# Kernel tuning notes

Measured on AMD Instinct MI355X. Metric: run time of the kernel, lower is better.

Reference implementation:

```python
import jax, jax.numpy as jnp
import numpy as np

IN_D = 4096
OUT_D = 4096
NNZ = 1677722
BATCH = 4096
NEG_SLOPE = 0.1


def setup_inputs() -> dict:
    key = jax.random.key(0)
    k_x, k_w, k_b, k_r, k_c = jax.random.split(key, 5)
    x = jax.random.normal(k_x, (BATCH, IN_D), dtype=jnp.float32)
    weight = jax.random.normal(k_w, (NNZ,), dtype=jnp.float32)
    bias = jax.random.normal(k_b, (OUT_D,), dtype=jnp.float32)
    rows = jax.random.randint(k_r, (NNZ,), 0, IN_D, dtype=jnp.int32)
    cols = jax.random.randint(k_c, (NNZ,), 0, OUT_D, dtype=jnp.int32)
    return {"x": x, "weight": weight, "bias": bias, "rows": rows, "cols": cols}


def reference(x, weight, bias, rows, cols):
    # Sparse.forward: W = zeros(in_d, out_d); W[loc] = weight; rho(bias + x @ W)
    W = jnp.zeros((IN_D, OUT_D), dtype=x.dtype).at[rows, cols].set(weight)
    return jax.nn.leaky_relu(bias + x @ W, negative_slope=NEG_SLOPE)
```

## Files before the change

### kernel.cpp

```cpp
#include <hip/hip_runtime.h>
#include <stdint.h>

#define IN_D  4096
#define OUT_D 4096
#define BATCH 4096
#define NEG_SLOPE 0.1f
#define NSEG 8
#define SEGCAP 192

typedef __attribute__((ext_vector_type(8))) short short8;
typedef __attribute__((ext_vector_type(4))) float f32x4;

__device__ __forceinline__ unsigned short f2bf(float f) {
    unsigned u = __builtin_bit_cast(unsigned, f);
    u += 0x7FFFu + ((u >> 16) & 1u);
    return (unsigned short)(u >> 16);
}

__device__ __forceinline__ void gload_lds16(const unsigned short* gsrc, unsigned short* ldsp) {
    __builtin_amdgcn_global_load_lds(
        (const __attribute__((address_space(1))) unsigned int*)gsrc,
        (__attribute__((address_space(3))) unsigned int*)ldsp,
        16, 0, 0);
}

__global__ void zerocnt_kernel(uint4* __restrict__ cnt4) {
    int i = blockIdx.x * blockDim.x + threadIdx.x;
    cnt4[i] = make_uint4(0u, 0u, 0u, 0u);
}

__global__ void bucketcvt_kernel(const int* __restrict__ rows, const int* __restrict__ cols,
                                 const float* __restrict__ w,
                                 unsigned* __restrict__ cnt, uint2* __restrict__ bucket,
                                 int nnz,
                                 const float4* __restrict__ x, ushort4* __restrict__ xb,
                                 int nx4) {
    const int stride = gridDim.x * blockDim.x;
    const int i0 = blockIdx.x * blockDim.x + threadIdx.x;
    const int g = blockIdx.x & (NSEG - 1);
    for (int i = i0; i < nnz; i += stride) {
        int c = cols[i];
        unsigned pos = atomicAdd(&cnt[g * OUT_D + c], 1u);
        if (pos < SEGCAP)
            bucket[((size_t)g * OUT_D + c) * SEGCAP + pos] =
                make_uint2((unsigned)rows[i] | ((unsigned)f2bf(w[i]) << 16),
                           (unsigned)(i + 1));
    }
    for (int i = i0; i < nx4; i += stride) {
        float4 v = x[i];
        ushort4 o;
        o.x = f2bf(v.x); o.y = f2bf(v.y); o.z = f2bf(v.z); o.w = f2bf(v.w);
        xb[i] = o;
    }
}

__global__ __launch_bounds__(256) void coldedup_kernel(
        const uint2* __restrict__ bucket, const unsigned* __restrict__ cnt,
        unsigned short* __restrict__ Wt) {
    __shared__ unsigned tag[IN_D];
    __shared__ unsigned short wv[IN_D];
    const int col = blockIdx.x;
    const int tid = threadIdx.x;

    for (int r = tid; r < IN_D; r += 256) tag[r] = 0u;
    __syncthreads();

    #pragma unroll
    for (int g = 0; g < NSEG; ++g) {
        const int n = min((int)cnt[g * OUT_D + col], SEGCAP);
        const uint2* bk = bucket + ((size_t)g * OUT_D + col) * SEGCAP;
        for (int e = tid; e < n; e += 256) {
            uint2 u = bk[e];
            atomicMax(&tag[u.x & 0xFFFu], u.y);
        }
    }
    __syncthreads();
    #pragma unroll
    for (int g = 0; g < NSEG; ++g) {
        const int n = min((int)cnt[g * OUT_D + col], SEGCAP);
        const uint2* bk = bucket + ((size_t)g * OUT_D + col) * SEGCAP;
        for (int e = tid; e < n; e += 256) {
            uint2 u = bk[e];
            if (tag[u.x & 0xFFFu] == u.y) wv[u.x & 0xFFFu] = (unsigned short)(u.x >> 16);
        }
    }
    __syncthreads();

    const int r0 = tid * 16;
    short8 o0, o1;
    #pragma unroll
    for (int j = 0; j < 8; ++j) {
        o0[j] = tag[r0 + j]     ? (short)wv[r0 + j]     : (short)0;
        o1[j] = tag[r0 + 8 + j] ? (short)wv[r0 + 8 + j] : (short)0;
    }
    *(short8*)&Wt[(size_t)col * IN_D + r0]     = o0;
    *(short8*)&Wt[(size_t)col * IN_D + r0 + 8] = o1;
}

#define BM 256
#define BN 256
#define BK 64
#define NT (IN_D / BK)

#define QUAD(MI0, NI0, BREG) \
    _Pragma("unroll") \
    for (int mi = 0; mi < 4; ++mi) { \
      _Pragma("unroll") \
      for (int ni = 0; ni < 2; ++ni) { \
        _Pragma("unroll") \
        for (int ks = 0; ks < 2; ++ks) { \
          acc[(MI0)+mi][(NI0)+ni] = __builtin_amdgcn_mfma_f32_16x16x32_bf16( \
              a[mi][ks], BREG[ni][ks], acc[(MI0)+mi][(NI0)+ni], 0, 0, 0); \
        } } }

#define PHASE_TAIL(QUADCALL) \
    __builtin_amdgcn_s_barrier(); \
    asm volatile("s_waitcnt lgkmcnt(0)" ::: "memory"); \
    __builtin_amdgcn_sched_barrier(0); \
    __builtin_amdgcn_s_setprio(1); \
    QUADCALL; \
    __builtin_amdgcn_s_setprio(0); \
    __builtin_amdgcn_s_barrier();

__global__ __launch_bounds__(512) void gemm_kernel(
        const unsigned short* __restrict__ Xb,
        const unsigned short* __restrict__ Wt,
        const float* __restrict__ bias,
        float* __restrict__ out)
{
    __shared__ unsigned short lds[2][2][2][128 * 64];

    const int tid  = threadIdx.x;
    const int lane = tid & 63;
    const int wave = tid >> 6;

    const int lin = blockIdx.y * 16 + blockIdx.x;
    const int swz = (lin & 7) * 32 + (lin >> 3);
    const int m0 = (swz >> 4) * BM;
    const int n0 = (swz & 15) * BN;

    const int wm = (wave >> 2) * 128;
    const int wn = (wave & 3) * 64;

    const int lr = lane & 15;
    const int kg = lane >> 4;
    const int x7 = lr & 7;
    const int l8 = lane >> 3;
    const int c8 = lane & 7;

    const int kp0 = ((0 * 4 + kg) ^ x7) * 8;
    const int kp1 = ((1 * 4 + kg) ^ x7) * 8;

    const int jA_base = (wave >> 2) * 64 + lr;
    int jB[4];
    #pragma unroll
    for (int ni = 0; ni < 4; ++ni) {
        int r16 = wn + ni * 16;
        jB[ni] = (r16 & 31) + ((r16 >> 6) << 5) + lr;
    }

    auto stageA = [&](int d, int h, int kt) {
        #pragma unroll
        for (int s = 0; s < 2; ++s) {
            int j = wave * 16 + s * 8 + l8;
            int trow = (j & 63) + h * 64 + ((j >> 6) << 7);
            const unsigned short* src =
                Xb + (size_t)(m0 + trow) * IN_D + kt * BK + 8 * (c8 ^ l8);
            gload_lds16(src, &lds[d][0][h][(wave * 16 + s * 8) * 64]);
        }
    };
    auto stageB = [&](int d, int h, int kt) {
        #pragma unroll
        for (int s = 0; s < 2; ++s) {
            int j = wave * 16 + s * 8 + l8;
            int trow = (j & 31) + h * 32 + ((j >> 5) << 6);
            const unsigned short* src =
                Wt + (size_t)(n0 + trow) * IN_D + kt * BK + 8 * (c8 ^ l8);
            gload_lds16(src, &lds[d][1][h][(wave * 16 + s * 8) * 64]);
        }
    };

    f32x4 acc[8][4] = {};
    short8 a[4][2], b0[2][2], b1[2][2];

    stageA(0, 0, 0); stageB(0, 0, 0); stageB(0, 1, 0); stageA(0, 1, 0);
    stageA(1, 0, 1); stageB(1, 1, 1); stageA(1, 1, 1);
    asm volatile("s_waitcnt vmcnt(6)" ::: "memory");
    __builtin_amdgcn_s_barrier();
    #pragma unroll
    for (int mi = 0; mi < 4; ++mi) {
        a[mi][0] = *(const short8*)&lds[0][0][0][(jA_base + mi * 16) * 64 + kp0];
        a[mi][1] = *(const short8*)&lds[0][0][0][(jA_base + mi * 16) * 64 + kp1];
    }
    b0[0][0] = *(const short8*)&lds[0][1][0][jB[0] * 64 + kp0];
    b0[0][1] = *(const short8*)&lds[0][1][0][jB[0] * 64 + kp1];
    b0[1][0] = *(const short8*)&lds[0][1][0][jB[1] * 64 + kp0];
    b0[1][1] = *(const short8*)&lds[0][1][0][jB[1] * 64 + kp1];

    for (int t = 0; t < NT; ++t) {
        const int cur = t & 1, nxt = cur ^ 1;
        const int kt1 = (t + 1) & (NT - 1);
        const int kt2 = (t + 2) & (NT - 1);

        stageB(nxt, 0, kt1);
        PHASE_TAIL(QUAD(0, 0, b0))

        b1[0][0] = *(const short8*)&lds[cur][1][1][jB[2] * 64 + kp0];
        b1[0][1] = *(const short8*)&lds[cur][1][1][jB[2] * 64 + kp1];
        b1[1][0] = *(const short8*)&lds[cur][1][1][jB[3] * 64 + kp0];
        b1[1][1] = *(const short8*)&lds[cur][1][1][jB[3] * 64 + kp1];
        stageA(cur, 0, kt2);
        PHASE_TAIL(QUAD(0, 2, b1))

        #pragma unroll
        for (int mi = 0; mi < 4; ++mi) {
            a[mi][0] = *(const short8*)&lds[cur][0][1][(jA_base + mi * 16) * 64 + kp0];
            a[mi][1] = *(const short8*)&lds[cur][0][1][(jA_base + mi * 16) * 64 + kp1];
        }
        stageB(cur, 1, kt2);
        PHASE_TAIL(QUAD(4, 2, b1))

        stageA(cur, 1, kt2);
        asm volatile("s_waitcnt vmcnt(6)" ::: "memory");
        __builtin_amdgcn_s_barrier();
        asm volatile("s_waitcnt lgkmcnt(0)" ::: "memory");
        __builtin_amdgcn_sched_barrier(0);
        __builtin_amdgcn_s_setprio(1);
        QUAD(4, 0, b0)
        __builtin_amdgcn_s_setprio(0);
        #pragma unroll
        for (int mi = 0; mi < 4; ++mi) {
            a[mi][0] = *(const short8*)&lds[nxt][0][0][(jA_base + mi * 16) * 64 + kp0];
            a[mi][1] = *(const short8*)&lds[nxt][0][0][(jA_base + mi * 16) * 64 + kp1];
        }
        b0[0][0] = *(const short8*)&lds[nxt][1][0][jB[0] * 64 + kp0];
        b0[0][1] = *(const short8*)&lds[nxt][1][0][jB[0] * 64 + kp1];
        b0[1][0] = *(const short8*)&lds[nxt][1][0][jB[1] * 64 + kp0];
        b0[1][1] = *(const short8*)&lds[nxt][1][0][jB[1] * 64 + kp1];
        __builtin_amdgcn_s_barrier();
    }

    float bfrag[4];
    #pragma unroll
    for (int ni = 0; ni < 4; ++ni) bfrag[ni] = bias[n0 + wn + ni * 16 + lr];

    #pragma unroll
    for (int mi = 0; mi < 8; ++mi) {
        #pragma unroll
        for (int ni = 0; ni < 4; ++ni) {
            const int col = n0 + wn + ni * 16 + lr;
            #pragma unroll
            for (int r = 0; r < 4; ++r) {
                const int row = m0 + wm + mi * 16 + kg * 4 + r;
                float v = acc[mi][ni][r] + bfrag[ni];
                v = v > 0.0f ? v : v * NEG_SLOPE;
                out[(size_t)row * OUT_D + col] = v;
            }
        }
    }
}

extern "C" void kernel_launch(void* const* d_in, const int* in_sizes, int n_in,
                              void* d_out, int out_size, void* d_ws, size_t ws_size,
                              hipStream_t stream) {
    const float* x    = (const float*)d_in[0];
    const float* w    = (const float*)d_in[1];
    const float* bias = (const float*)d_in[2];
    const int*   rows = (const int*)d_in[3];
    const int*   cols = (const int*)d_in[4];
    const int nnz = in_sizes[1];
    float* out = (float*)d_out;

    const size_t NW = (size_t)IN_D * OUT_D;
    unsigned*        cnt    = (unsigned*)d_ws;
    uint2*           bucket = (uint2*)((char*)d_ws + (1u << 20));
    unsigned short*  Wt     = (unsigned short*)((char*)d_ws + (1u << 20)
                                  + (size_t)NSEG * OUT_D * SEGCAP * 8);
    unsigned short*  Xb     = (unsigned short*)((char*)Wt + NW * 2);

    zerocnt_kernel<<<32, 256, 0, stream>>>((uint4*)cnt);
    bucketcvt_kernel<<<2048, 256, 0, stream>>>(rows, cols, w, cnt, bucket, nnz,
                                               (const float4*)x, (ushort4*)Xb,
                                               (int)((size_t)BATCH * IN_D / 4));
    coldedup_kernel<<<OUT_D, 256, 0, stream>>>(bucket, cnt, Wt);

    dim3 grid(OUT_D / BN, BATCH / BM);
    gemm_kernel<<<grid, 512, 0, stream>>>(Xb, Wt, bias, out);
}
```

Before: 217.9 us.

## Single-pass packed atomicMax dedup and rotate GEMM pipeline phases

The column dedup kernel now packs the entry index and bf16 weight into a 64-bit LDS tag and uses one 64-bit atomicMax pass. This removes the second bucket scan and the separate weight array. The GEMM main loop is rotated so the first quadrant's MFMAs run at the end of the previous iteration, with a peeled prologue and epilogue. That moves the stageB issue and removes one barrier pair per K-step. The risk is that 64-bit LDS atomics cost more than 32-bit ones, and the reordered waitcnt and barrier placement must stay race-free.

```diff
diff --git a/kernel.cpp b/kernel.cpp
--- a/kernel.cpp
+++ b/kernel.cpp
@@ -57,12 +57,13 @@
 __global__ __launch_bounds__(256) void coldedup_kernel(
         const uint2* __restrict__ bucket, const unsigned* __restrict__ cnt,
         unsigned short* __restrict__ Wt) {
-    __shared__ unsigned tag[IN_D];
-    __shared__ unsigned short wv[IN_D];
+    __shared__ unsigned long long tag[IN_D];
     const int col = blockIdx.x;
     const int tid = threadIdx.x;
 
-    for (int r = tid; r < IN_D; r += 256) tag[r] = 0u;
+    uint4* t4 = (uint4*)tag;
+    #pragma unroll
+    for (int j = 0; j < 8; ++j) t4[tid + j * 256] = make_uint4(0u, 0u, 0u, 0u);
     __syncthreads();
 
     #pragma unroll
@@ -71,17 +72,8 @@
         const uint2* bk = bucket + ((size_t)g * OUT_D + col) * SEGCAP;
         for (int e = tid; e < n; e += 256) {
             uint2 u = bk[e];
-            atomicMax(&tag[u.x & 0xFFFu], u.y);
-        }
-    }
-    __syncthreads();
-    #pragma unroll
-    for (int g = 0; g < NSEG; ++g) {
-        const int n = min((int)cnt[g * OUT_D + col], SEGCAP);
-        const uint2* bk = bucket + ((size_t)g * OUT_D + col) * SEGCAP;
-        for (int e = tid; e < n; e += 256) {
-            uint2 u = bk[e];
-            if (tag[u.x & 0xFFFu] == u.y) wv[u.x & 0xFFFu] = (unsigned short)(u.x >> 16);
+            unsigned long long v = ((unsigned long long)u.y << 16) | (u.x >> 16);
+            atomicMax(&tag[u.x & 0xFFFu], v);
         }
     }
     __syncthreads();
@@ -90,8 +82,8 @@
     short8 o0, o1;
     #pragma unroll
     for (int j = 0; j < 8; ++j) {
-        o0[j] = tag[r0 + j]     ? (short)wv[r0 + j]     : (short)0;
-        o1[j] = tag[r0 + 8 + j] ? (short)wv[r0 + 8 + j] : (short)0;
+        o0[j] = (short)(unsigned short)(tag[r0 + j] & 0xFFFFu);
+        o1[j] = (short)(unsigned short)(tag[r0 + 8 + j] & 0xFFFFu);
     }
     *(short8*)&Wt[(size_t)col * IN_D + r0]     = o0;
     *(short8*)&Wt[(size_t)col * IN_D + r0 + 8] = o1;
@@ -122,6 +114,17 @@
     __builtin_amdgcn_s_setprio(0); \
     __builtin_amdgcn_s_barrier();
 
+#define PREFETCH(D) \
+    _Pragma("unroll") \
+    for (int mi = 0; mi < 4; ++mi) { \
+        a[mi][0] = *(const short8*)&lds[D][0][0][(jA_base + mi * 16) * 64 + kp0]; \
+        a[mi][1] = *(const short8*)&lds[D][0][0][(jA_base + mi * 16) * 64 + kp1]; \
+    } \
+    b0[0][0] = *(const short8*)&lds[D][1][0][jB[0] * 64 + kp0]; \
+    b0[0][1] = *(const short8*)&lds[D][1][0][jB[0] * 64 + kp1]; \
+    b0[1][0] = *(const short8*)&lds[D][1][0][jB[1] * 64 + kp0]; \
+    b0[1][1] = *(const short8*)&lds[D][1][0][jB[1] * 64 + kp1];
+
 __global__ __launch_bounds__(512) void gemm_kernel(
         const unsigned short* __restrict__ Xb,
         const unsigned short* __restrict__ Wt,
@@ -184,26 +187,20 @@
     short8 a[4][2], b0[2][2], b1[2][2];
 
     stageA(0, 0, 0); stageB(0, 0, 0); stageB(0, 1, 0); stageA(0, 1, 0);
-    stageA(1, 0, 1); stageB(1, 1, 1); stageA(1, 1, 1);
-    asm volatile("s_waitcnt vmcnt(6)" ::: "memory");
+    stageA(1, 0, 1); stageB(1, 1, 1); stageA(1, 1, 1); stageB(1, 0, 1);
+    asm volatile("s_waitcnt vmcnt(8)" ::: "memory");
     __builtin_amdgcn_s_barrier();
-    #pragma unroll
-    for (int mi = 0; mi < 4; ++mi) {
-        a[mi][0] = *(const short8*)&lds[0][0][0][(jA_base + mi * 16) * 64 + kp0];
-        a[mi][1] = *(const short8*)&lds[0][0][0][(jA_base + mi * 16) * 64 + kp1];
-    }
-    b0[0][0] = *(const short8*)&lds[0][1][0][jB[0] * 64 + kp0];
-    b0[0][1] = *(const short8*)&lds[0][1][0][jB[0] * 64 + kp1];
-    b0[1][0] = *(const short8*)&lds[0][1][0][jB[1] * 64 + kp0];
-    b0[1][1] = *(const short8*)&lds[0][1][0][jB[1] * 64 + kp1];
-
-    for (int t = 0; t < NT; ++t) {
+    PREFETCH(0)
+    asm volatile("s_waitcnt lgkmcnt(0)" ::: "memory");
+    __builtin_amdgcn_sched_barrier(0);
+    __builtin_amdgcn_s_setprio(1);
+    QUAD(0, 0, b0)
+    __builtin_amdgcn_s_setprio(0);
+    __builtin_amdgcn_s_barrier();
+
+    for (int t = 0; t < NT - 1; ++t) {
         const int cur = t & 1, nxt = cur ^ 1;
-        const int kt1 = (t + 1) & (NT - 1);
         const int kt2 = (t + 2) & (NT - 1);
-
-        stageB(nxt, 0, kt1);
-        PHASE_TAIL(QUAD(0, 0, b0))
 
         b1[0][0] = *(const short8*)&lds[cur][1][1][jB[2] * 64 + kp0];
         b1[0][1] = *(const short8*)&lds[cur][1][1][jB[2] * 64 + kp1];
@@ -228,16 +225,34 @@
         __builtin_amdgcn_s_setprio(1);
         QUAD(4, 0, b0)
         __builtin_amdgcn_s_setprio(0);
+        PREFETCH(nxt)
+        stageB(cur, 0, kt2);
+        asm volatile("s_waitcnt lgkmcnt(0)" ::: "memory");
+        __builtin_amdgcn_sched_barrier(0);
+        __builtin_amdgcn_s_setprio(1);
+        QUAD(0, 0, b0)
+        __builtin_amdgcn_s_setprio(0);
+        __builtin_amdgcn_s_barrier();
+    }
+
+    {
+        const int cur = (NT - 1) & 1;
+        b1[0][0] = *(const short8*)&lds[cur][1][1][jB[2] * 64 + kp0];
+        b1[0][1] = *(const short8*)&lds[cur][1][1][jB[2] * 64 + kp1];
+        b1[1][0] = *(const short8*)&lds[cur][1][1][jB[3] * 64 + kp0];
+        b1[1][1] = *(const short8*)&lds[cur][1][1][jB[3] * 64 + kp1];
+        PHASE_TAIL(QUAD(0, 2, b1))
         #pragma unroll
         for (int mi = 0; mi < 4; ++mi) {
-            a[mi][0] = *(const short8*)&lds[nxt][0][0][(jA_base + mi * 16) * 64 + kp0];
-            a[mi][1] = *(const short8*)&lds[nxt][0][0][(jA_base + mi * 16) * 64 + kp1];
-        }
-        b0[0][0] = *(const short8*)&lds[nxt][1][0][jB[0] * 64 + kp0];
-        b0[0][1] = *(const short8*)&lds[nxt][1][0][jB[0] * 64 + kp1];
-        b0[1][0] = *(const short8*)&lds[nxt][1][0][jB[1] * 64 + kp0];
-        b0[1][1] = *(const short8*)&lds[nxt][1][0][jB[1] * 64 + kp1];
-        __builtin_amdgcn_s_barrier();
+            a[mi][0] = *(const short8*)&lds[cur][0][1][(jA_base + mi * 16) * 64 + kp0];
+            a[mi][1] = *(const short8*)&lds[cur][0][1][(jA_base + mi * 16) * 64 + kp1];
+        }
+        asm volatile("s_waitcnt lgkmcnt(0)" ::: "memory");
+        __builtin_amdgcn_sched_barrier(0);
+        __builtin_amdgcn_s_setprio(1);
+        QUAD(4, 2, b1)
+        QUAD(4, 0, b0)
+        __builtin_amdgcn_s_setprio(0);
     }
 
     float bfrag[4];
```

Measured after the change: 204.8 us. -6.0%, faster.
